# Kernel optimization log

Measured on AMD Instinct MI355X. Metric: run time of the kernel, lower is better.

Reference implementation:

```python
import jax, jax.numpy as jnp
import numpy as np

B, S, H = 4, 2048, 1024  # batch, seq, hidden


def setup_inputs() -> dict:
    key = jax.random.key(0)
    kq, kk, kv = jax.random.split(key, 3)
    return {
        "Q": jax.random.normal(kq, (B, S, H), dtype=jnp.float32),
        "K": jax.random.normal(kk, (B, S, H), dtype=jnp.float32),
        "V": jax.random.normal(kv, (B, S, H), dtype=jnp.float32),
    }


def reference(Q, K, V):
    # Phase of rfft along hidden dim -> [B, S, F], F = H//2 + 1
    q_fft = jnp.fft.rfft(Q, axis=-1)
    k_fft = jnp.fft.rfft(K, axis=-1)
    q_phase = jnp.arctan2(q_fft.imag, q_fft.real)
    k_phase = jnp.arctan2(k_fft.imag, k_fft.real)
    n_freqs = q_phase.shape[-1]
    # mean_f cos(qp_i - kp_j) = (cos(qp) @ cos(kp)^T + sin(qp) @ sin(kp)^T) / F
    # Avoids materializing the [B,S,S,F] phase_diff tensor; math is identical.
    align = (
        jnp.einsum("bif,bjf->bij", jnp.cos(q_phase), jnp.cos(k_phase))
        + jnp.einsum("bif,bjf->bij", jnp.sin(q_phase), jnp.sin(k_phase))
    ) / n_freqs
    scores = align + 1.0
    weights = jax.nn.softmax(scores, axis=-1)  # [B, S, S]
    output = jnp.einsum("bij,bjh->bih", weights, V)  # [B, S, H]
    return output, weights
```

## Files before the change

### kernel.cpp

```cpp
#include <hip/hip_runtime.h>
#include <hip/hip_bf16.h>
#include <math.h>

#define Bb 4
#define Ss 2048
#define Hh 1024
#define Ff 513
#define FEAT 1026
#define KP2 1088

typedef __attribute__((ext_vector_type(8))) short bf16x8;
typedef __attribute__((ext_vector_type(4))) float f32x4;
typedef __attribute__((ext_vector_type(16))) float f32x16;

typedef const __attribute__((address_space(1))) void GVoid;
typedef __attribute__((address_space(3))) void LVoid;

#define PADI(i) ((i) + ((i) >> 4))

__device__ __forceinline__ float2 cmul(float2 a, float2 b) {
  return make_float2(a.x * b.x - a.y * b.y, a.x * b.y + a.y * b.x);
}

__device__ __forceinline__ unsigned short bf16bits(float x) {
  __hip_bfloat16 h = __float2bfloat16(x);
  return *reinterpret_cast<unsigned short*>(&h);
}

__device__ __forceinline__ bf16x8 lds_read_b128(const short* p) {
  bf16x8 r;
  asm volatile("ds_read_b128 %0, %1"
               : "=&v"(r)
               : "v"((const __attribute__((address_space(3))) short*)p));
  return r;
}

__global__ __launch_bounds__(256) void fft_phase_kernel(
    const float* __restrict__ Q, const float* __restrict__ Kin,
    __hip_bfloat16* __restrict__ FQ, __hip_bfloat16* __restrict__ FK) {
  const int row = blockIdx.x;
  const float* qs = Q   + (size_t)row * Hh;
  const float* ks = Kin + (size_t)row * Hh;
  __hip_bfloat16* fq = FQ + (size_t)row * KP2;
  __hip_bfloat16* fk = FK + (size_t)row * KP2;

  __shared__ float2 data[PADI(1023) + 1];
  __shared__ float2 tw[1024];
  const int tid = threadIdx.x;

#pragma unroll
  for (int e = 0; e < 4; ++e) {
    const int m = tid + e * 256;
    float s, c;
    sincosf(-6.283185307179586f * (float)m * (1.0f / 1024.0f), &s, &c);
    tw[m] = make_float2(c, s);
  }
#pragma unroll
  for (int e = 0; e < 4; ++e) {
    const int n = tid + e * 256;
    const int r4 = ((n & 3) << 8) | (((n >> 2) & 3) << 6) | (((n >> 4) & 3) << 4)
                 | (((n >> 6) & 3) << 2) | ((n >> 8) & 3);
    data[PADI(r4)] = make_float2(qs[n], ks[n]);
  }
  __syncthreads();

  int quarter = 1, step = 256;
  for (int s = 0; s < 5; ++s) {
    const int j = tid & (quarter - 1);
    const int pos = 4 * tid - 3 * j;
    const float2 x0 = data[PADI(pos)];
    const float2 x1 = data[PADI(pos + quarter)];
    const float2 x2 = data[PADI(pos + 2 * quarter)];
    const float2 x3 = data[PADI(pos + 3 * quarter)];
    const int e1 = j * step;
    const float2 a1 = cmul(x1, tw[e1]);
    const float2 a2 = cmul(x2, tw[2 * e1]);
    const float2 a3 = cmul(x3, tw[3 * e1]);
    const float2 t0 = make_float2(x0.x + a2.x, x0.y + a2.y);
    const float2 t1 = make_float2(x0.x - a2.x, x0.y - a2.y);
    const float2 t2 = make_float2(a1.x + a3.x, a1.y + a3.y);
    const float2 t3 = make_float2(a1.x - a3.x, a1.y - a3.y);
    data[PADI(pos)]               = make_float2(t0.x + t2.x, t0.y + t2.y);
    data[PADI(pos + quarter)]     = make_float2(t1.x + t3.y, t1.y - t3.x);
    data[PADI(pos + 2 * quarter)] = make_float2(t0.x - t2.x, t0.y - t2.y);
    data[PADI(pos + 3 * quarter)] = make_float2(t1.x - t3.y, t1.y + t3.x);
    __syncthreads();
    quarter <<= 2; step >>= 2;
  }

  for (int f = tid; f <= 512; f += 256) {
    const float2 z1 = data[PADI(f)];
    const float2 z2 = data[PADI((1024 - f) & 1023)];
    const float qr = z1.x + z2.x, qi = z1.y - z2.y;
    const float kr = z1.y + z2.y, ki = z2.x - z1.x;
    float qc, qsn, kc, ksn;
    const float qm2 = qr * qr + qi * qi;
    if (qm2 > 1e-30f) { const float iv = rsqrtf(qm2); qc = qr * iv; qsn = qi * iv; }
    else              { qc = 1.0f; qsn = 0.0f; }
    const float km2 = kr * kr + ki * ki;
    if (km2 > 1e-30f) { const float iv = rsqrtf(km2); kc = kr * iv; ksn = ki * iv; }
    else              { kc = 1.0f; ksn = 0.0f; }
    fq[f] = __float2bfloat16(qc); fq[Ff + f] = __float2bfloat16(qsn);
    fk[f] = __float2bfloat16(kc); fk[Ff + f] = __float2bfloat16(ksn);
  }
  for (int p = FEAT + tid; p < KP2; p += 256) {
    fq[p] = __float2bfloat16(0.0f);
    fk[p] = __float2bfloat16(0.0f);
  }
}

__global__ __launch_bounds__(256) void vt_kernel(
    const float* __restrict__ V, __hip_bfloat16* __restrict__ Vt) {
  const int b = blockIdx.z;
  const int h0 = blockIdx.x * 32;
  const int s0 = blockIdx.y * 32;
  __shared__ float t[32][33];
  const int tid = threadIdx.x;
  const int c = tid & 31;
  const int r8 = tid >> 5;
  const float* Vb = V + (size_t)b * Ss * Hh;
#pragma unroll
  for (int e = 0; e < 4; ++e) {
    const int r = r8 + e * 8;
    t[r][c] = Vb[(size_t)(s0 + r) * Hh + h0 + c];
  }
  __syncthreads();
  __hip_bfloat16* O = Vt + (size_t)b * Hh * Ss;
#pragma unroll
  for (int e = 0; e < 4; ++e) {
    const int hh = r8 + e * 8;
    O[(size_t)(h0 + hh) * Ss + s0 + c] = __float2bfloat16(t[c][hh]);
  }
}

template<int K, int LDA, int LDB, int LDC, int EPI, int BMT>
__global__ __launch_bounds__(512, 2) void gemm32(
    const __hip_bfloat16* __restrict__ Ag, const __hip_bfloat16* __restrict__ Bg,
    float* __restrict__ Cg, size_t strA, size_t strB, size_t strC) {
  constexpr int nt  = K / 64;
  constexpr int MF  = BMT / 64;
  constexpr int SAW = BMT / 128;

  const int gx = gridDim.x, gy = gridDim.y;
  const int nwg = gx * gy * (int)gridDim.z;
  int f = ((int)blockIdx.z * gy + (int)blockIdx.y) * gx + (int)blockIdx.x;
  f = (f & 7) * (nwg >> 3) + (f >> 3);
  const int bx = f % gx; f /= gx;
  const int by = f % gy;
  const int bz = f / gy;

  const int i0 = by * BMT;
  const int j0 = bx * 256;
  const char* Ab = (const char*)(Ag + (size_t)bz * strA);
  const char* Bp = (const char*)(Bg + (size_t)bz * strB);
  float* C = Cg + (size_t)bz * strC;

  __shared__ short As[2][BMT * 64];
  __shared__ short Bs[2][256 * 64];

  const int tid = threadIdx.x;
  const int lane = tid & 63;
  const int w  = tid >> 6;
  const int wm = w >> 2;
  const int wn = w & 3;

  f32x16 acc[MF][2];
#pragma unroll
  for (int mi = 0; mi < MF; ++mi)
#pragma unroll
    for (int ni = 0; ni < 2; ++ni)
#pragma unroll
      for (int r = 0; r < 16; ++r) acc[mi][ni][r] = 0.0f;

#define BAR() __builtin_amdgcn_s_barrier()
#define WAITDEEP()                                                                       \
  do {                                                                                   \
    if constexpr (SAW == 2) asm volatile("s_waitcnt vmcnt(8)");                          \
    else                    asm volatile("s_waitcnt vmcnt(6)");                          \
  } while (0)

#define SA(dd, tt, kh)                                                                   \
  do {                                                                                   \
    _Pragma("unroll")                                                                    \
    for (int ii = 0; ii < SAW; ++ii) {                                                   \
      const int f_ = w * SAW + ii;                                                       \
      const int rg_ = f_ >> 1;                                                           \
      const int kc_ = 2 * (kh) + (f_ & 1);                                               \
      __builtin_amdgcn_global_load_lds(                                                  \
          (GVoid*)(Ab + (size_t)(i0 + rg_ * 32 + (lane & 31)) * (LDA * 2) +              \
                   (size_t)(tt) * 128 + kc_ * 32 + (lane >> 5) * 16),                    \
          (LVoid*)&As[dd][(rg_ * 4 + kc_) * 512], 16, 0, 0);                             \
    }                                                                                    \
  } while (0)
#define SB(dd, tt, kh)                                                                   \
  do {                                                                                   \
    _Pragma("unroll")                                                                    \
    for (int ii = 0; ii < 2; ++ii) {                                                     \
      const int f_ = w * 2 + ii;                                                         \
      const int rg_ = f_ >> 1;                                                           \
      const int kc_ = 2 * (kh) + (f_ & 1);                                               \
      __builtin_amdgcn_global_load_lds(                                                  \
          (GVoid*)(Bp + (size_t)(j0 + rg_ * 32 + (lane & 31)) * (LDB * 2) +              \
                   (size_t)(tt) * 128 + kc_ * 32 + (lane >> 5) * 16),                    \
          (LVoid*)&Bs[dd][(rg_ * 4 + kc_) * 512], 16, 0, 0);                             \
    }                                                                                    \
  } while (0)
#define RA(dd, kh)                                                                       \
  _Pragma("unroll")                                                                      \
  for (int mi = 0; mi < MF; ++mi)                                                        \
    _Pragma("unroll")                                                                    \
    for (int kb = 0; kb < 2; ++kb)                                                       \
      af[mi][kb] = lds_read_b128(                                                        \
          &As[dd][((wm * MF + mi) * 4 + 2 * (kh) + kb) * 512 + lane * 8]);
#define RB(dd, kh)                                                                       \
  _Pragma("unroll")                                                                      \
  for (int ni = 0; ni < 2; ++ni)                                                         \
    _Pragma("unroll")                                                                    \
    for (int kb = 0; kb < 2; ++kb)                                                       \
      bf[ni][kb] = lds_read_b128(                                                        \
          &Bs[dd][((wn * 2 + ni) * 4 + 2 * (kh) + kb) * 512 + lane * 8]);
#define MM()                                                                             \
  asm volatile("s_waitcnt lgkmcnt(0)");                                                  \
  __builtin_amdgcn_sched_barrier(0);                                                     \
  __builtin_amdgcn_s_setprio(1);                                                         \
  _Pragma("unroll")                                                                      \
  for (int mi = 0; mi < MF; ++mi)                                                        \
    _Pragma("unroll")                                                                    \
    for (int ni = 0; ni < 2; ++ni)                                                       \
      _Pragma("unroll")                                                                  \
      for (int kb = 0; kb < 2; ++kb)                                                     \
        acc[mi][ni] = __builtin_amdgcn_mfma_f32_32x32x16_bf16(                           \
            af[mi][kb], bf[ni][kb], acc[mi][ni], 0, 0, 0);                               \
  __builtin_amdgcn_s_setprio(0);                                                         \
  __builtin_amdgcn_sched_barrier(0);

  SA(0, 0, 0); SB(0, 0, 0);
  SA(0, 0, 1); SB(0, 0, 1);
  SA(1, 1, 0); SB(1, 1, 0);
  WAITDEEP();
  BAR();

  for (int t = 0; t < nt; ++t) {
    const int d = t & 1;
    bf16x8 af[MF][2], bf[2][2];

    RA(d, 0); RB(d, 0);
    if (t + 1 < nt) { SA(d ^ 1, t + 1, 1); SB(d ^ 1, t + 1, 1); }
    MM();
    if (t + 2 < nt) WAITDEEP();
    else            asm volatile("s_waitcnt vmcnt(0)");
    BAR();

    RA(d, 1); RB(d, 1);
    if (t + 2 < nt) { SA(d, t + 2, 0); SB(d, t + 2, 0); }
    MM();
    if (t + 2 < nt) WAITDEEP();
    else            asm volatile("s_waitcnt vmcnt(0)");
    BAR();
  }
#undef SA
#undef SB
#undef RA
#undef RB
#undef MM
#undef WAITDEEP
#undef BAR

  const int col = lane & 31;
  const int rbase = (lane >> 5) * 4;
#pragma unroll
  for (int mi = 0; mi < MF; ++mi) {
#pragma unroll
    for (int ni = 0; ni < 2; ++ni) {
#pragma unroll
      for (int r = 0; r < 16; ++r) {
        const int row = (r & 3) + 8 * (r >> 2) + rbase;
        const int i = i0 + wm * (MF * 32) + mi * 32 + row;
        const int j = j0 + wn * 64 + ni * 32 + col;
        float v = acc[mi][ni][r];
        if (EPI == 0) v *= (1.0f / 513.0f);
        C[(size_t)i * LDC + j] = v;
      }
    }
  }
}

__global__ __launch_bounds__(256) void softmax_kernel(
    float* __restrict__ W, __hip_bfloat16* __restrict__ Wb) {
  const size_t row = blockIdx.x;
  float* p = W + row * (size_t)Ss;
  __hip_bfloat16* pb = Wb + row * (size_t)Ss;
  const int tid = threadIdx.x;
  __shared__ float red[4];

  const float4* p4 = (const float4*)p;
  const float4 a = p4[2 * tid];
  const float4 bq = p4[2 * tid + 1];
  float v[8] = {a.x, a.y, a.z, a.w, bq.x, bq.y, bq.z, bq.w};

  float m = v[0];
#pragma unroll
  for (int e = 1; e < 8; ++e) m = fmaxf(m, v[e]);
#pragma unroll
  for (int off = 32; off > 0; off >>= 1) m = fmaxf(m, __shfl_xor(m, off, 64));
  if ((tid & 63) == 0) red[tid >> 6] = m;
  __syncthreads();
  m = fmaxf(fmaxf(red[0], red[1]), fmaxf(red[2], red[3]));

  float sum = 0.0f;
#pragma unroll
  for (int e = 0; e < 8; ++e) { v[e] = __expf(v[e] - m); sum += v[e]; }
#pragma unroll
  for (int off = 32; off > 0; off >>= 1) sum += __shfl_xor(sum, off, 64);
  __syncthreads();
  if ((tid & 63) == 0) red[tid >> 6] = sum;
  __syncthreads();
  sum = red[0] + red[1] + red[2] + red[3];

  const float rs = 1.0f / sum;
#pragma unroll
  for (int e = 0; e < 8; ++e) v[e] *= rs;

  float4* o4 = (float4*)p;
  o4[2 * tid]     = make_float4(v[0], v[1], v[2], v[3]);
  o4[2 * tid + 1] = make_float4(v[4], v[5], v[6], v[7]);

  bf16x8 ob;
#pragma unroll
  for (int e = 0; e < 8; ++e) ob[e] = (short)bf16bits(v[e]);
  *(bf16x8*)&pb[8 * tid] = ob;
}

extern "C" void kernel_launch(void* const* d_in, const int* in_sizes, int n_in,
                              void* d_out, int out_size, void* d_ws, size_t ws_size,
                              hipStream_t stream) {
  const float* Q = (const float*)d_in[0];
  const float* K = (const float*)d_in[1];
  const float* V = (const float*)d_in[2];

  float* out     = (float*)d_out;
  float* weights = out + (size_t)Bb * Ss * Hh;

  __hip_bfloat16* FQb = (__hip_bfloat16*)d_ws;
  __hip_bfloat16* FKb = FQb + (size_t)Bb * Ss * KP2;
  __hip_bfloat16* Vtb = FKb + (size_t)Bb * Ss * KP2;
  __hip_bfloat16* Wb  = (__hip_bfloat16*)d_ws;

  hipLaunchKernelGGL(fft_phase_kernel, dim3(Bb * Ss), dim3(256), 0, stream,
                     Q, K, FQb, FKb);
  hipLaunchKernelGGL(vt_kernel, dim3(Hh / 32, Ss / 32, Bb), dim3(256), 0, stream,
                     V, Vtb);
  hipLaunchKernelGGL((gemm32<KP2, KP2, KP2, Ss, 0, 256>), dim3(Ss / 256, Ss / 256, Bb),
                     dim3(512), 0, stream, FQb, FKb, weights,
                     (size_t)Ss * KP2, (size_t)Ss * KP2, (size_t)Ss * Ss);
  hipLaunchKernelGGL(softmax_kernel, dim3(Bb * Ss), dim3(256), 0, stream,
                     weights, Wb);
  hipLaunchKernelGGL((gemm32<Ss, Ss, Ss, Hh, 1, 128>), dim3(Hh / 256, Ss / 128, Bb),
                     dim3(512), 0, stream, Wb, Vtb, out,
                     (size_t)Ss * Ss, (size_t)Hh * Ss, (size_t)Ss * Hh);
}
```

Before: 169.5 us.

## Drop zero sine features to shrink GEMM K dimension and unify GEMM tiling

For real input, the sine of the phase is exactly zero at the DC and Nyquist bins. The phase kernel therefore packs 513 cosines plus 511 sines into exactly 1024 bf16 features. This drops both the zero padding up to 1088 and the padding writes, which shortens the K loop of the alignment GEMM. The FFT input load is vectorised to float4. The GEMM template loses its BMT parameter, so the weights×V GEMM now uses 256-row tiles. That halves its workgroup count to 128, which may underfill the GPU's compute units.

```diff
diff --git a/kernel.cpp b/kernel.cpp
--- a/kernel.cpp
+++ b/kernel.cpp
@@ -6,11 +6,9 @@
 #define Ss 2048
 #define Hh 1024
 #define Ff 513
-#define FEAT 1026
-#define KP2 1088
+#define KP2 1024
 
 typedef __attribute__((ext_vector_type(8))) short bf16x8;
-typedef __attribute__((ext_vector_type(4))) float f32x4;
 typedef __attribute__((ext_vector_type(16))) float f32x16;
 
 typedef const __attribute__((address_space(1))) void GVoid;
@@ -55,12 +53,16 @@
     sincosf(-6.283185307179586f * (float)m * (1.0f / 1024.0f), &s, &c);
     tw[m] = make_float2(c, s);
   }
-#pragma unroll
-  for (int e = 0; e < 4; ++e) {
-    const int n = tid + e * 256;
-    const int r4 = ((n & 3) << 8) | (((n >> 2) & 3) << 6) | (((n >> 4) & 3) << 4)
-                 | (((n >> 6) & 3) << 2) | ((n >> 8) & 3);
-    data[PADI(r4)] = make_float2(qs[n], ks[n]);
+  {
+    const float4 qv = ((const float4*)qs)[tid];
+    const float4 kv = ((const float4*)ks)[tid];
+#pragma unroll
+    for (int j = 0; j < 4; ++j) {
+      const int n = 4 * tid + j;
+      const int r4 = ((n & 3) << 8) | (((n >> 2) & 3) << 6) | (((n >> 4) & 3) << 4)
+                   | (((n >> 6) & 3) << 2) | ((n >> 8) & 3);
+      data[PADI(r4)] = make_float2(((const float*)&qv)[j], ((const float*)&kv)[j]);
+    }
   }
   __syncthreads();
 
@@ -100,12 +102,12 @@
     const float km2 = kr * kr + ki * ki;
     if (km2 > 1e-30f) { const float iv = rsqrtf(km2); kc = kr * iv; ksn = ki * iv; }
     else              { kc = 1.0f; ksn = 0.0f; }
-    fq[f] = __float2bfloat16(qc); fq[Ff + f] = __float2bfloat16(qsn);
-    fk[f] = __float2bfloat16(kc); fk[Ff + f] = __float2bfloat16(ksn);
-  }
-  for (int p = FEAT + tid; p < KP2; p += 256) {
-    fq[p] = __float2bfloat16(0.0f);
-    fk[p] = __float2bfloat16(0.0f);
+    fq[f] = __float2bfloat16(qc);
+    fk[f] = __float2bfloat16(kc);
+    if (f > 0 && f < 512) {
+      fq[512 + f] = __float2bfloat16(qsn);
+      fk[512 + f] = __float2bfloat16(ksn);
+    }
   }
 }
 
@@ -133,13 +135,12 @@
   }
 }
 
-template<int K, int LDA, int LDB, int LDC, int EPI, int BMT>
+template<int K, int LDA, int LDB, int LDC, int EPI>
 __global__ __launch_bounds__(512, 2) void gemm32(
     const __hip_bfloat16* __restrict__ Ag, const __hip_bfloat16* __restrict__ Bg,
     float* __restrict__ Cg, size_t strA, size_t strB, size_t strC) {
-  constexpr int nt  = K / 64;
-  constexpr int MF  = BMT / 64;
-  constexpr int SAW = BMT / 128;
+  constexpr int nt = K / 64;
+  constexpr int MF = 4;
 
   const int gx = gridDim.x, gy = gridDim.y;
   const int nwg = gx * gy * (int)gridDim.z;
@@ -149,14 +150,14 @@
   const int by = f % gy;
   const int bz = f / gy;
 
-  const int i0 = by * BMT;
+  const int i0 = by * 256;
   const int j0 = bx * 256;
   const char* Ab = (const char*)(Ag + (size_t)bz * strA);
   const char* Bp = (const char*)(Bg + (size_t)bz * strB);
   float* C = Cg + (size_t)bz * strC;
 
-  __shared__ short As[2][BMT * 64];
-  __shared__ short Bs[2][256 * 64];
+  __shared__ short As[2][16384];
+  __shared__ short Bs[2][16384];
 
   const int tid = threadIdx.x;
   const int lane = tid & 63;
@@ -173,17 +174,13 @@
       for (int r = 0; r < 16; ++r) acc[mi][ni][r] = 0.0f;
 
 #define BAR() __builtin_amdgcn_s_barrier()
-#define WAITDEEP()                                                                       \
-  do {                                                                                   \
-    if constexpr (SAW == 2) asm volatile("s_waitcnt vmcnt(8)");                          \
-    else                    asm volatile("s_waitcnt vmcnt(6)");                          \
-  } while (0)
+#define WAITDEEP() asm volatile("s_waitcnt vmcnt(8)")
 
 #define SA(dd, tt, kh)                                                                   \
   do {                                                                                   \
     _Pragma("unroll")                                                                    \
-    for (int ii = 0; ii < SAW; ++ii) {                                                   \
-      const int f_ = w * SAW + ii;                                                       \
+    for (int ii = 0; ii < 2; ++ii) {                                                     \
+      const int f_ = w * 2 + ii;                                                         \
       const int rg_ = f_ >> 1;                                                           \
       const int kc_ = 2 * (kh) + (f_ & 1);                                               \
       __builtin_amdgcn_global_load_lds(                                                  \
@@ -275,7 +272,7 @@
 #pragma unroll
       for (int r = 0; r < 16; ++r) {
         const int row = (r & 3) + 8 * (r >> 2) + rbase;
-        const int i = i0 + wm * (MF * 32) + mi * 32 + row;
+        const int i = i0 + wm * 128 + mi * 32 + row;
         const int j = j0 + wn * 64 + ni * 32 + col;
         float v = acc[mi][ni][r];
         if (EPI == 0) v *= (1.0f / 513.0f);
@@ -350,12 +347,12 @@
                      Q, K, FQb, FKb);
   hipLaunchKernelGGL(vt_kernel, dim3(Hh / 32, Ss / 32, Bb), dim3(256), 0, stream,
                      V, Vtb);
-  hipLaunchKernelGGL((gemm32<KP2, KP2, KP2, Ss, 0, 256>), dim3(Ss / 256, Ss / 256, Bb),
+  hipLaunchKernelGGL((gemm32<KP2, KP2, KP2, Ss, 0>), dim3(Ss / 256, Ss / 256, Bb),
                      dim3(512), 0, stream, FQb, FKb, weights,
                      (size_t)Ss * KP2, (size_t)Ss * KP2, (size_t)Ss * Ss);
   hipLaunchKernelGGL(softmax_kernel, dim3(Bb * Ss), dim3(256), 0, stream,
                      weights, Wb);
-  hipLaunchKernelGGL((gemm32<Ss, Ss, Ss, Hh, 1, 128>), dim3(Hh / 256, Ss / 128, Bb),
+  hipLaunchKernelGGL((gemm32<Ss, Ss, Ss, Hh, 1>), dim3(Hh / 256, Ss / 256, Bb),
                      dim3(512), 0, stream, Wb, Vtb, out,
                      (size_t)Ss * Ss, (size_t)Hh * Ss, (size_t)Ss * Hh);
 }
```

Result: slower. 180.8 us (+6.7%).
